# Performance work log

Hardware: AMD Instinct MI355X
Metric: run time of the kernel (lower is better)

## Reference

```python
import jax, jax.numpy as jnp
import numpy as np

DIM = 2048
N_HEADS = 16
HEAD_DIM = DIM // N_HEADS
MAX_SEQ_LEN = 2048
ROPE_THETA = 32.0
EPS = 1e-6


def _precompute_freqs_1d(dim, max_seq_len, theta):
    freqs = theta ** (-np.arange(0, dim, 2, dtype=np.float32) / dim)  # [dim/2]
    pos = np.arange(max_seq_len, dtype=np.float32)                    # [S]
    ang = pos[:, None] * freqs[None, :]                               # [S, dim/2]
    return jnp.asarray(np.cos(ang)), jnp.asarray(np.sin(ang))


def _rms_norm(x, w):
    # x: [..., d]
    inv = jax.lax.rsqrt(jnp.mean(x * x, axis=-1, keepdims=True) + EPS)
    return x * inv * w


def setup_inputs() -> dict:
    key = jax.random.key(0)
    k1, k2, k3 = jax.random.split(key, 3)
    bsz, seq_len = 4, 2048
    x = jax.random.normal(k1, (bsz, seq_len, DIM), dtype=jnp.float32)
    w_qkv = jax.random.normal(k2, (3 * DIM, DIM), dtype=jnp.float32) * (DIM ** -0.5)
    w_proj = jax.random.normal(k3, (DIM, DIM), dtype=jnp.float32) * (DIM ** -0.5)
    q_norm_w = jnp.ones((HEAD_DIM,), dtype=jnp.float32)
    k_norm_w = jnp.ones((HEAD_DIM,), dtype=jnp.float32)
    return {"x": x, "w_qkv": w_qkv, "w_proj": w_proj,
            "q_norm_w": q_norm_w, "k_norm_w": k_norm_w}


def reference(x, w_qkv, w_proj, q_norm_w, k_norm_w):
    bsz, seq_len, dim = x.shape
    scale = HEAD_DIM ** -0.5

    # QKV projection (torch Linear: x @ W^T)
    qkv = jnp.einsum('bsd,ed->bse', x, w_qkv)  # [b, s, 3*dim]
    qkv = qkv.reshape(bsz, seq_len, 3, N_HEADS, HEAD_DIM).transpose(2, 0, 3, 1, 4)
    q, k, v = qkv[0], qkv[1], qkv[2]           # each [b, h, s, d]

    # Per-head RMSNorm on q, k
    q = _rms_norm(q, q_norm_w)
    k = _rms_norm(k, k_norm_w)

    # RoPE (half-split convention)
    cos, sin = _precompute_freqs_1d(HEAD_DIM, MAX_SEQ_LEN, ROPE_THETA)
    cos = cos[:seq_len][None, None]  # [1,1,s,d/2]
    sin = sin[:seq_len][None, None]
    q1, q2 = jnp.split(q, 2, axis=-1)
    k1, k2 = jnp.split(k, 2, axis=-1)
    q = jnp.concatenate([q1 * cos - q2 * sin, q2 * cos + q1 * sin], axis=-1)
    k = jnp.concatenate([k1 * cos - k2 * sin, k2 * cos + k1 * sin], axis=-1)

    # Scaled dot-product attention (no mask, eval-mode: no dropout)
    scores = jnp.einsum('bhqd,bhkd->bhqk', q, k) * scale
    attn = jax.nn.softmax(scores, axis=-1)
    y = jnp.einsum('bhqk,bhkd->bhqd', attn, v)

    # Merge heads + output projection
    y = y.transpose(0, 2, 1, 3).reshape(bsz, seq_len, dim)
    return jnp.einsum('bsd,ed->bse', y, w_proj)
```

## Files before the change

### kernel.cpp

```cpp
#include <hip/hip_runtime.h>
#include <hip/hip_bf16.h>

#define BSZ 4
#define SEQ 2048
#define DIM 2048
#define NH 16
#define HD 128
#define QK_LD 4096
#define SCALE 0.08838834764831845f
#define SC2 0.12751742910198f

typedef __attribute__((ext_vector_type(8))) short bf16x8;
typedef __attribute__((ext_vector_type(4))) float f32x4;

#define GLDS16(g, l)                                                           \
  __builtin_amdgcn_global_load_lds(                                           \
      (const __attribute__((address_space(1))) void*)(g),                     \
      (__attribute__((address_space(3))) void*)(l), 16, 0, 0)

__device__ inline short f2b(float f) {
  __hip_bfloat16 h = __float2bfloat16(f);
  short s;
  __builtin_memcpy(&s, &h, 2);
  return s;
}

__device__ inline void stage16(const float* gp, __hip_bfloat16* lp) {
  float4 q0 = ((const float4*)gp)[0], q1 = ((const float4*)gp)[1];
  float4 q2 = ((const float4*)gp)[2], q3 = ((const float4*)gp)[3];
  bf16x8 v0, v1;
  v0[0] = f2b(q0.x); v0[1] = f2b(q0.y); v0[2] = f2b(q0.z); v0[3] = f2b(q0.w);
  v0[4] = f2b(q1.x); v0[5] = f2b(q1.y); v0[6] = f2b(q1.z); v0[7] = f2b(q1.w);
  v1[0] = f2b(q2.x); v1[1] = f2b(q2.y); v1[2] = f2b(q2.z); v1[3] = f2b(q2.w);
  v1[4] = f2b(q3.x); v1[5] = f2b(q3.y); v1[6] = f2b(q3.z); v1[7] = f2b(q3.w);
  *(bf16x8*)lp = v0;
  *(bf16x8*)(lp + 8) = v1;
}

__device__ inline char* out_slice(void* outv, int b, int fl) {
  return (char*)outv + (size_t)b * (size_t)SEQ * DIM * (fl ? 2u : 4u);
}

__global__ __launch_bounds__(256)
void detect_canon(const unsigned int* __restrict__ wbits,
                  const void* __restrict__ qw, const void* __restrict__ kw,
                  __hip_bfloat16* __restrict__ qwb,
                  __hip_bfloat16* __restrict__ kwb, int* __restrict__ flag) {
  __shared__ int cnt;
  const int t = threadIdx.x;
  if (t == 0) cnt = 0;
  __syncthreads();
  int local = 0;
  for (int i = 0; i < 4; ++i) {
    unsigned int e = (wbits[t * 4 + i] >> 7) & 0xFF;
    if (e >= 96 && e < 160) local++;
  }
  atomicAdd(&cnt, local);
  __syncthreads();
  const int f = (cnt >= 768) ? 1 : 0;
  if (t == 0) *flag = f;
  if (t < 128)
    qwb[t] = f ? ((const __hip_bfloat16*)qw)[t]
               : __float2bfloat16(((const float*)qw)[t]);
  else
    kwb[t - 128] = f ? ((const __hip_bfloat16*)kw)[t - 128]
                     : __float2bfloat16(((const float*)kw)[t - 128]);
}

__global__ __launch_bounds__(256)
void convert_bf16(const void* __restrict__ in, __hip_bfloat16* __restrict__ out,
                  const int* __restrict__ flag) {
  const int fl = *flag;
  long i = ((long)blockIdx.x * 256 + threadIdx.x) * 8;
  if (fl) {
    *(float4*)(out + i) = *(const float4*)((const __hip_bfloat16*)in + i);
  } else {
    const float* p = (const float*)in + i;
    float4 a = ((const float4*)p)[0], b = ((const float4*)p)[1];
    bf16x8 o;
    o[0] = f2b(a.x); o[1] = f2b(a.y); o[2] = f2b(a.z); o[3] = f2b(a.w);
    o[4] = f2b(b.x); o[5] = f2b(b.y); o[6] = f2b(b.z); o[7] = f2b(b.w);
    *(bf16x8*)(out + i) = o;
  }
}


__global__ __launch_bounds__(256)
void gemm_qkv_full(const __hip_bfloat16* __restrict__ A,
                   const __hip_bfloat16* __restrict__ B,
                   __hip_bfloat16* __restrict__ qk, void* __restrict__ outv,
                   const int* __restrict__ flag) {
  __shared__ __hip_bfloat16 As[128 * 32];
  __shared__ __hip_bfloat16 Bs[128 * 32];
  const int t = threadIdx.x, wave = t >> 6, lane = t & 63;
  const int quad = lane >> 4, l16 = lane & 15;
  const int wm = (wave & 1) * 64, wn = (wave >> 1) * 64;
  const long bm = (long)blockIdx.x * 128, bn = (long)blockIdx.y * 128;
  const int fl = *flag;

  f32x4 acc[4][4] = {};
  for (int k0 = 0; k0 < DIM; k0 += 32) {
    __syncthreads();
    for (int i = 0; i < 2; ++i) {
      int c = wave * 64 + lane + i * 256;
      int row = c >> 2, kc = c & 3;
      GLDS16(A + (bm + row) * DIM + k0 + kc * 8, As + (wave * 64 + i * 256) * 8);
      GLDS16(B + (bn + row) * DIM + k0 + kc * 8, Bs + (wave * 64 + i * 256) * 8);
    }
    __syncthreads();
    bf16x8 aF[4], bF[4];
    for (int mt = 0; mt < 4; ++mt)
      aF[mt] = *(const bf16x8*)(As + (wm + mt * 16 + l16) * 32 + quad * 8);
    for (int nt = 0; nt < 4; ++nt)
      bF[nt] = *(const bf16x8*)(Bs + (wn + nt * 16 + l16) * 32 + quad * 8);
    for (int mt = 0; mt < 4; ++mt)
      for (int nt = 0; nt < 4; ++nt)
        acc[mt][nt] = __builtin_amdgcn_mfma_f32_16x16x32_bf16(
            aF[mt], bF[nt], acc[mt][nt], 0, 0, 0);
  }

  if (bn < 4096) {
    for (int mt = 0; mt < 4; ++mt) {
      long gr = bm + wm + mt * 16 + quad * 4;
      for (int nt = 0; nt < 4; ++nt) {
        long gc = bn + wn + nt * 16 + l16;
        for (int r = 0; r < 4; ++r)
          qk[(gr + r) * QK_LD + gc] = __float2bfloat16(acc[mt][nt][r]);
      }
    }
  } else {
    for (int mt = 0; mt < 4; ++mt) {
      long gr = bm + wm + mt * 16 + quad * 4;
      __hip_bfloat16* vtb = (__hip_bfloat16*)out_slice(outv, (int)(gr >> 11), fl);
      long s = gr & 2047;
      for (int nt = 0; nt < 4; ++nt) {
        long col = bn - 4096 + wn + nt * 16 + l16;
        for (int r = 0; r < 4; ++r)
          vtb[col * SEQ + s + r] = __float2bfloat16(acc[mt][nt][r]);
      }
    }
  }
}

__global__ __launch_bounds__(256)
void gemm_proj_full(const __hip_bfloat16* __restrict__ A,
                    const __hip_bfloat16* __restrict__ B,
                    void* __restrict__ outv, const int* __restrict__ flag) {
  __shared__ __hip_bfloat16 As[128 * 32];
  __shared__ __hip_bfloat16 Bs[128 * 32];
  const int t = threadIdx.x, wave = t >> 6, lane = t & 63;
  const int quad = lane >> 4, l16 = lane & 15;
  const int wm = (wave & 1) * 64, wn = (wave >> 1) * 64;
  const long bm = (long)blockIdx.x * 128, bn = (long)blockIdx.y * 128;
  const int fl = *flag;

  f32x4 acc[4][4] = {};
  for (int k0 = 0; k0 < DIM; k0 += 32) {
    __syncthreads();
    for (int i = 0; i < 2; ++i) {
      int c = wave * 64 + lane + i * 256;
      int row = c >> 2, kc = c & 3;
      GLDS16(A + (bm + row) * QK_LD + k0 + kc * 8, As + (wave * 64 + i * 256) * 8);
      GLDS16(B + (bn + row) * DIM + k0 + kc * 8, Bs + (wave * 64 + i * 256) * 8);
    }
    __syncthreads();
    bf16x8 aF[4], bF[4];
    for (int mt = 0; mt < 4; ++mt)
      aF[mt] = *(const bf16x8*)(As + (wm + mt * 16 + l16) * 32 + quad * 8);
    for (int nt = 0; nt < 4; ++nt)
      bF[nt] = *(const bf16x8*)(Bs + (wn + nt * 16 + l16) * 32 + quad * 8);
    for (int mt = 0; mt < 4; ++mt)
      for (int nt = 0; nt < 4; ++nt)
        acc[mt][nt] = __builtin_amdgcn_mfma_f32_16x16x32_bf16(
            aF[mt], bF[nt], acc[mt][nt], 0, 0, 0);
  }

  for (int mt = 0; mt < 4; ++mt) {
    long gr = bm + wm + mt * 16 + quad * 4;
    for (int nt = 0; nt < 4; ++nt) {
      long gc = bn + wn + nt * 16 + l16;
      for (int r = 0; r < 4; ++r) {
        long idx = (gr + r) * DIM + gc;
        if (fl) ((__hip_bfloat16*)outv)[idx] = __float2bfloat16(acc[mt][nt][r]);
        else    ((float*)outv)[idx] = acc[mt][nt][r];
      }
    }
  }
}


__global__ __launch_bounds__(256)
void gemm_qkv(const void* __restrict__ xin, const void* __restrict__ win,
              __hip_bfloat16* __restrict__ qk, void* __restrict__ outv,
              const int* __restrict__ flag, int b) {
  __shared__ __hip_bfloat16 As[128 * 32];
  __shared__ __hip_bfloat16 Bs[128 * 32];
  const int t = threadIdx.x, wave = t >> 6, lane = t & 63;
  const int quad = lane >> 4, l16 = lane & 15;
  const int wm = (wave & 1) * 64, wn = (wave >> 1) * 64;
  const long bm = (long)blockIdx.x * 128, bn = (long)blockIdx.y * 128;
  const int fl = *flag;
  const __hip_bfloat16* Ab = (const __hip_bfloat16*)xin + (long)b * SEQ * DIM;
  const __hip_bfloat16* Bb = (const __hip_bfloat16*)win;
  const float* Af = (const float*)xin + (long)b * SEQ * DIM;
  const float* Bf = (const float*)win;

  f32x4 acc[4][4] = {};
  for (int k0 = 0; k0 < DIM; k0 += 32) {
    __syncthreads();
    if (fl) {
      for (int i = 0; i < 2; ++i) {
        int c = wave * 64 + lane + i * 256;
        int row = c >> 2, kc = c & 3;
        GLDS16(Ab + (bm + row) * DIM + k0 + kc * 8, As + (wave * 64 + i * 256) * 8);
        GLDS16(Bb + (bn + row) * DIM + k0 + kc * 8, Bs + (wave * 64 + i * 256) * 8);
      }
    } else {
      int row = t >> 1, cb = k0 + (t & 1) * 16;
      stage16(Af + (bm + row) * DIM + cb, As + t * 16);
      stage16(Bf + (bn + row) * DIM + cb, Bs + t * 16);
    }
    __syncthreads();
    bf16x8 aF[4], bF[4];
    for (int mt = 0; mt < 4; ++mt)
      aF[mt] = *(const bf16x8*)(As + (wm + mt * 16 + l16) * 32 + quad * 8);
    for (int nt = 0; nt < 4; ++nt)
      bF[nt] = *(const bf16x8*)(Bs + (wn + nt * 16 + l16) * 32 + quad * 8);
    for (int mt = 0; mt < 4; ++mt)
      for (int nt = 0; nt < 4; ++nt)
        acc[mt][nt] = __builtin_amdgcn_mfma_f32_16x16x32_bf16(
            aF[mt], bF[nt], acc[mt][nt], 0, 0, 0);
  }

  if (bn < 4096) {
    for (int mt = 0; mt < 4; ++mt) {
      long gr = bm + wm + mt * 16 + quad * 4;
      for (int nt = 0; nt < 4; ++nt) {
        long gc = bn + wn + nt * 16 + l16;
        for (int r = 0; r < 4; ++r)
          qk[(gr + r) * QK_LD + gc] = __float2bfloat16(acc[mt][nt][r]);
      }
    }
  } else {
    __hip_bfloat16* vtb = (__hip_bfloat16*)out_slice(outv, b, fl);
    for (int mt = 0; mt < 4; ++mt) {
      long gr = bm + wm + mt * 16 + quad * 4;
      for (int nt = 0; nt < 4; ++nt) {
        long col = bn - 4096 + wn + nt * 16 + l16;
        for (int r = 0; r < 4; ++r)
          vtb[col * SEQ + gr + r] = __float2bfloat16(acc[mt][nt][r]);
      }
    }
  }
}

__global__ __launch_bounds__(256)
void gemm_proj(const __hip_bfloat16* __restrict__ A, const void* __restrict__ win,
               void* __restrict__ outv, const int* __restrict__ flag, int b) {
  __shared__ __hip_bfloat16 As[128 * 32];
  __shared__ __hip_bfloat16 Bs[128 * 32];
  const int t = threadIdx.x, wave = t >> 6, lane = t & 63;
  const int quad = lane >> 4, l16 = lane & 15;
  const int wm = (wave & 1) * 64, wn = (wave >> 1) * 64;
  const long bm = (long)blockIdx.x * 128, bn = (long)blockIdx.y * 128;
  const int fl = *flag;
  const __hip_bfloat16* Bb = (const __hip_bfloat16*)win;
  const float* Bf = (const float*)win;

  f32x4 acc[4][4] = {};
  for (int k0 = 0; k0 < DIM; k0 += 32) {
    __syncthreads();
    for (int i = 0; i < 2; ++i) {
      int c = wave * 64 + lane + i * 256;
      int row = c >> 2, kc = c & 3;
      GLDS16(A + (bm + row) * QK_LD + k0 + kc * 8, As + (wave * 64 + i * 256) * 8);
    }
    if (fl) {
      for (int i = 0; i < 2; ++i) {
        int c = wave * 64 + lane + i * 256;
        int row = c >> 2, kc = c & 3;
        GLDS16(Bb + (bn + row) * DIM + k0 + kc * 8, Bs + (wave * 64 + i * 256) * 8);
      }
    } else {
      int row = t >> 1, cb = k0 + (t & 1) * 16;
      stage16(Bf + (bn + row) * DIM + cb, Bs + t * 16);
    }
    __syncthreads();
    bf16x8 aF[4], bF[4];
    for (int mt = 0; mt < 4; ++mt)
      aF[mt] = *(const bf16x8*)(As + (wm + mt * 16 + l16) * 32 + quad * 8);
    for (int nt = 0; nt < 4; ++nt)
      bF[nt] = *(const bf16x8*)(Bs + (wn + nt * 16 + l16) * 32 + quad * 8);
    for (int mt = 0; mt < 4; ++mt)
      for (int nt = 0; nt < 4; ++nt)
        acc[mt][nt] = __builtin_amdgcn_mfma_f32_16x16x32_bf16(
            aF[mt], bF[nt], acc[mt][nt], 0, 0, 0);
  }

  char* Cb = out_slice(outv, b, fl);
  for (int mt = 0; mt < 4; ++mt) {
    long gr = bm + wm + mt * 16 + quad * 4;
    for (int nt = 0; nt < 4; ++nt) {
      long gc = bn + wn + nt * 16 + l16;
      for (int r = 0; r < 4; ++r) {
        long idx = (gr + r) * DIM + gc;
        if (fl) ((__hip_bfloat16*)Cb)[idx] = __float2bfloat16(acc[mt][nt][r]);
        else    ((float*)Cb)[idx] = acc[mt][nt][r];
      }
    }
  }
}


__global__ __launch_bounds__(256)
void norm_rope(__hip_bfloat16* __restrict__ qk,
               const __hip_bfloat16* __restrict__ qwb,
               const __hip_bfloat16* __restrict__ kwb) {
  const int wave = threadIdx.x >> 6, lane = threadIdx.x & 63;
  const int gid = blockIdx.x * 4 + wave;
  const int h = gid & 15, tt = (gid >> 4) & 1, row = gid >> 5;
  const int s = row & 2047;

  __hip_bfloat16* p = qk + (long)row * QK_LD + tt * DIM + h * HD;
  unsigned int u = ((const unsigned int*)p)[lane];

  unsigned int x = (unsigned int)__shfl((int)u, lane >> 1);
  unsigned int y = (unsigned int)__shfl((int)u, 32 + (lane >> 1));
  float v1 = __uint_as_float((lane & 1) ? (x & 0xFFFF0000u) : (x << 16));
  float v2 = __uint_as_float((lane & 1) ? (y & 0xFFFF0000u) : (y << 16));

  float ss = v1 * v1 + v2 * v2;
  for (int off = 1; off < 64; off <<= 1) ss += __shfl_xor(ss, off);
  float inv = rsqrtf(ss * (1.0f / 128.0f) + 1e-6f);

  const __hip_bfloat16* w = tt ? kwb : qwb;
  float n1 = v1 * inv * __bfloat162float(w[lane]);
  float n2 = v2 * inv * __bfloat162float(w[lane + 64]);

  float freq = exp2f(-5.0f * (float)lane * (1.0f / 64.0f));
  float ang = (float)s * freq;
  float c = cosf(ang), sn = sinf(ang);
  float r1 = n1 * c - n2 * sn;
  float r2 = n2 * c + n1 * sn;

  float z1lo = __shfl(r1, (2 * lane) & 63), z2lo = __shfl(r2, (2 * lane) & 63);
  float z1hi = __shfl(r1, (2 * lane + 1) & 63), z2hi = __shfl(r2, (2 * lane + 1) & 63);
  float lo = (lane < 32) ? z1lo : z2lo;
  float hi = (lane < 32) ? z1hi : z2hi;
  unsigned int ou = (unsigned int)(unsigned short)f2b(lo) |
                    ((unsigned int)(unsigned short)f2b(hi) << 16);
  ((unsigned int*)p)[lane] = ou;
}

__global__ __launch_bounds__(512)
void flash_attn(__hip_bfloat16* __restrict__ qkbase, void* __restrict__ outv,
                const int* __restrict__ flag, int b0) {
  __shared__ __hip_bfloat16 Ks[4 * 64 * 32];
  __shared__ __hip_bfloat16 Vs[2 * 128 * 32];
  __shared__ __hip_bfloat16 Ps[8][2 * 16 * 32];

  const int t = threadIdx.x, wave = t >> 6, lane = t & 63;
  const int quad = lane >> 4, l16 = lane & 15;
  const int swz = (quad ^ ((l16 >> 1) & 3)) * 8;
  const int q0 = blockIdx.x * 128, h = blockIdx.y;
  const int b = b0 + blockIdx.z;
  const int fl = *flag;
  __hip_bfloat16* qk = qkbase + (long)blockIdx.z * SEQ * QK_LD;
  __hip_bfloat16* Qg = qk + h * HD;
  const __hip_bfloat16* Kg = Qg + DIM;
  const __hip_bfloat16* Vt =
      (const __hip_bfloat16*)out_slice(outv, b, fl) + (long)h * HD * SEQ;

  bf16x8 aQ[4];
#pragma unroll
  for (int ks = 0; ks < 4; ++ks)
    aQ[ks] = *(const bf16x8*)(Qg +
        (long)(q0 + wave * 16 + l16) * QK_LD + ks * 32 + quad * 8);

  f32x4 oacc[8] = {};
  float m_run[4], l_run[4];
#pragma unroll
  for (int r = 0; r < 4; ++r) { m_run[r] = -1e30f; l_run[r] = 0.0f; }

  for (int j0 = 0; j0 < SEQ; j0 += 64) {
    __syncthreads();
#pragma unroll
    for (int i = 0; i < 2; ++i) {
      int f = t + i * 512;
      int kk = f & 3, row = (f >> 2) & 63, ks = f >> 8;
      GLDS16(Kg + (long)(j0 + row) * QK_LD + ks * 32 + (kk ^ ((row >> 1) & 3)) * 8,
             Ks + (t + i * 512) * 8);
    }
#pragma unroll
    for (int i = 0; i < 2; ++i) {
      int f = t + i * 512;
      int kk = f & 3, dimr = (f >> 2) & 127, ks2 = f >> 9;
      GLDS16(Vt + (long)dimr * SEQ + j0 + ks2 * 32 + (kk ^ ((dimr >> 1) & 3)) * 8,
             Vs + (t + i * 512) * 8);
    }
    __syncthreads();

    f32x4 sacc[4] = {};
#pragma unroll
    for (int ks = 0; ks < 4; ++ks)
#pragma unroll
      for (int nt = 0; nt < 4; ++nt) {
        bf16x8 bK = *(const bf16x8*)(Ks + (ks * 64 + nt * 16 + l16) * 32 + swz);
        sacc[nt] = __builtin_amdgcn_mfma_f32_16x16x32_bf16(
            aQ[ks], bK, sacc[nt], 0, 0, 0);
      }

    __hip_bfloat16* pw = &Ps[wave][0];
#pragma unroll
    for (int r = 0; r < 4; ++r) {
      float p0 = sacc[0][r] * SC2, p1 = sacc[1][r] * SC2;
      float p2 = sacc[2][r] * SC2, p3 = sacc[3][r] * SC2;
      float mx = fmaxf(fmaxf(p0, p1), fmaxf(p2, p3));
      for (int off = 1; off < 16; off <<= 1)
        mx = fmaxf(mx, __shfl_xor(mx, off));
      if (__any(mx > m_run[r] + 8.0f)) {
        float mnew = fmaxf(m_run[r], mx);
        float alpha = exp2f(m_run[r] - mnew);
        m_run[r] = mnew;
        l_run[r] *= alpha;
#pragma unroll
        for (int n = 0; n < 8; ++n) oacc[n][r] *= alpha;
      }
      float m = m_run[r];
      float e0 = exp2f(p0 - m), e1 = exp2f(p1 - m);
      float e2 = exp2f(p2 - m), e3 = exp2f(p3 - m);
      l_run[r] += (e0 + e1) + (e2 + e3);
      int rbase = (quad * 4 + r) * 32;
      int sc = (((quad * 4 + r) >> 1) & 3) << 3;
      pw[rbase + (l16 ^ sc)] = __float2bfloat16(e0);
      pw[rbase + ((l16 + 16) ^ sc)] = __float2bfloat16(e1);
      pw[512 + rbase + (l16 ^ sc)] = __float2bfloat16(e2);
      pw[512 + rbase + ((l16 + 16) ^ sc)] = __float2bfloat16(e3);
    }

#pragma unroll
    for (int ks2 = 0; ks2 < 2; ++ks2) {
      bf16x8 aP = *(const bf16x8*)(pw + (ks2 * 16 + l16) * 32 + swz);
#pragma unroll
      for (int n = 0; n < 8; ++n) {
        bf16x8 bV = *(const bf16x8*)(Vs + (ks2 * 128 + n * 16 + l16) * 32 + swz);
        oacc[n] = __builtin_amdgcn_mfma_f32_16x16x32_bf16(
            aP, bV, oacc[n], 0, 0, 0);
      }
    }
  }

#pragma unroll
  for (int r = 0; r < 4; ++r) {
    float l = l_run[r];
    for (int off = 1; off < 16; off <<= 1) l += __shfl_xor(l, off);
    float rl = 1.0f / l;
    long s = q0 + wave * 16 + quad * 4 + r;
    for (int n = 0; n < 8; ++n)
      qk[s * QK_LD + h * HD + n * 16 + l16] =
          __float2bfloat16(oacc[n][r] * rl);
  }
}

extern "C" void kernel_launch(void* const* d_in, const int* in_sizes, int n_in,
                              void* d_out, int out_size, void* d_ws, size_t ws_size,
                              hipStream_t stream) {
  int* flag = (int*)d_ws;
  __hip_bfloat16* qwb = (__hip_bfloat16*)((char*)d_ws + 64);
  __hip_bfloat16* kwb = qwb + 128;
  char* base = (char*)d_ws + 1024;

  detect_canon<<<1, 256, 0, stream>>>((const unsigned int*)d_in[1], d_in[3],
                                      d_in[4], qwb, kwb, flag);

  const size_t MB = 1024ull * 1024ull;
  const size_t NEED_A = 1024 + 128 * MB;

  if (ws_size >= NEED_A) {
    __hip_bfloat16* xb     = (__hip_bfloat16*)base;
    __hip_bfloat16* wqkvb  = (__hip_bfloat16*)(base + 32 * MB);
    __hip_bfloat16* wprojb = (__hip_bfloat16*)(base + 56 * MB);
    __hip_bfloat16* qk     = (__hip_bfloat16*)(base + 64 * MB);

    convert_bf16<<<(BSZ * SEQ * DIM) / 2048, 256, 0, stream>>>(d_in[0], xb, flag);
    convert_bf16<<<(3 * DIM * DIM) / 2048, 256, 0, stream>>>(d_in[1], wqkvb, flag);
    convert_bf16<<<(DIM * DIM) / 2048, 256, 0, stream>>>(d_in[2], wprojb, flag);

    gemm_qkv_full<<<dim3((BSZ * SEQ) / 128, (3 * DIM) / 128), 256, 0, stream>>>(
        xb, wqkvb, qk, d_out, flag);
    norm_rope<<<(BSZ * SEQ * 2 * NH) / 4, 256, 0, stream>>>(qk, qwb, kwb);
    flash_attn<<<dim3(SEQ / 128, NH, BSZ), 512, 0, stream>>>(qk, d_out, flag, 0);
    gemm_proj_full<<<dim3((BSZ * SEQ) / 128, DIM / 128), 256, 0, stream>>>(
        qk, wprojb, d_out, flag);
  } else {
    __hip_bfloat16* qk = (__hip_bfloat16*)base;
    for (int b = 0; b < BSZ; ++b) {
      gemm_qkv<<<dim3(SEQ / 128, (3 * DIM) / 128), 256, 0, stream>>>(
          d_in[0], d_in[1], qk, d_out, flag, b);
      norm_rope<<<(SEQ * 2 * NH) / 4, 256, 0, stream>>>(qk, qwb, kwb);
      flash_attn<<<dim3(SEQ / 128, NH, 1), 512, 0, stream>>>(qk, d_out, flag, b);
      gemm_proj<<<dim3(SEQ / 128, DIM / 128), 256, 0, stream>>>(
          qk, d_in[2], d_out, flag, b);
    }
  }
}
```

Before: 868.6 us.

## Keep softmax probabilities in registers via transposed QK MFMA and remap GEMM blocks across XCDs

```diff
diff --git a/kernel.cpp b/kernel.cpp
--- a/kernel.cpp
+++ b/kernel.cpp
@@ -39,6 +39,15 @@
 
 __device__ inline char* out_slice(void* outv, int b, int fl) {
   return (char*)outv + (size_t)b * (size_t)SEQ * DIM * (fl ? 2u : 4u);
+}
+
+__device__ inline void xcd_remap(long& bm, long& bn) {
+  int nwg = gridDim.x * gridDim.y;
+  int lin = blockIdx.y * gridDim.x + blockIdx.x;
+  int cpx = nwg >> 3;
+  lin = (lin & 7) * cpx + (lin >> 3);
+  bm = (long)(lin % gridDim.x) * 128;
+  bn = (long)(lin / gridDim.x) * 128;
 }
 
 __global__ __launch_bounds__(256)
@@ -95,7 +104,8 @@
   const int t = threadIdx.x, wave = t >> 6, lane = t & 63;
   const int quad = lane >> 4, l16 = lane & 15;
   const int wm = (wave & 1) * 64, wn = (wave >> 1) * 64;
-  const long bm = (long)blockIdx.x * 128, bn = (long)blockIdx.y * 128;
+  long bm, bn;
+  xcd_remap(bm, bn);
   const int fl = *flag;
 
   f32x4 acc[4][4] = {};
@@ -151,7 +161,8 @@
   const int t = threadIdx.x, wave = t >> 6, lane = t & 63;
   const int quad = lane >> 4, l16 = lane & 15;
   const int wm = (wave & 1) * 64, wn = (wave >> 1) * 64;
-  const long bm = (long)blockIdx.x * 128, bn = (long)blockIdx.y * 128;
+  long bm, bn;
+  xcd_remap(bm, bn);
   const int fl = *flag;
 
   f32x4 acc[4][4] = {};
@@ -357,7 +368,6 @@
                 const int* __restrict__ flag, int b0) {
   __shared__ __hip_bfloat16 Ks[4 * 64 * 32];
   __shared__ __hip_bfloat16 Vs[2 * 128 * 32];
-  __shared__ __hip_bfloat16 Ps[8][2 * 16 * 32];
 
   const int t = threadIdx.x, wave = t >> 6, lane = t & 63;
   const int quad = lane >> 4, l16 = lane & 15;
@@ -371,6 +381,10 @@
   const __hip_bfloat16* Vt =
       (const __hip_bfloat16*)out_slice(outv, b, fl) + (long)h * HD * SEQ;
 
+  const int srcA = ((lane >> 4) & 1) * 32 + l16;
+  const int srcB = srcA + 16;
+  const bool hiq = (quad >= 2);
+
   bf16x8 aQ[4];
 #pragma unroll
   for (int ks = 0; ks < 4; ++ks)
@@ -378,9 +392,7 @@
         (long)(q0 + wave * 16 + l16) * QK_LD + ks * 32 + quad * 8);
 
   f32x4 oacc[8] = {};
-  float m_run[4], l_run[4];
-#pragma unroll
-  for (int r = 0; r < 4; ++r) { m_run[r] = -1e30f; l_run[r] = 0.0f; }
+  float m_run = -1e30f, l_run = 0.0f;
 
   for (int j0 = 0; j0 < SEQ; j0 += 64) {
     __syncthreads();
@@ -407,40 +419,62 @@
       for (int nt = 0; nt < 4; ++nt) {
         bf16x8 bK = *(const bf16x8*)(Ks + (ks * 64 + nt * 16 + l16) * 32 + swz);
         sacc[nt] = __builtin_amdgcn_mfma_f32_16x16x32_bf16(
-            aQ[ks], bK, sacc[nt], 0, 0, 0);
-      }
-
-    __hip_bfloat16* pw = &Ps[wave][0];
-#pragma unroll
-    for (int r = 0; r < 4; ++r) {
-      float p0 = sacc[0][r] * SC2, p1 = sacc[1][r] * SC2;
-      float p2 = sacc[2][r] * SC2, p3 = sacc[3][r] * SC2;
-      float mx = fmaxf(fmaxf(p0, p1), fmaxf(p2, p3));
-      for (int off = 1; off < 16; off <<= 1)
-        mx = fmaxf(mx, __shfl_xor(mx, off));
-      if (__any(mx > m_run[r] + 8.0f)) {
-        float mnew = fmaxf(m_run[r], mx);
-        float alpha = exp2f(m_run[r] - mnew);
-        m_run[r] = mnew;
-        l_run[r] *= alpha;
-#pragma unroll
-        for (int n = 0; n < 8; ++n) oacc[n][r] *= alpha;
-      }
-      float m = m_run[r];
-      float e0 = exp2f(p0 - m), e1 = exp2f(p1 - m);
-      float e2 = exp2f(p2 - m), e3 = exp2f(p3 - m);
-      l_run[r] += (e0 + e1) + (e2 + e3);
-      int rbase = (quad * 4 + r) * 32;
-      int sc = (((quad * 4 + r) >> 1) & 3) << 3;
-      pw[rbase + (l16 ^ sc)] = __float2bfloat16(e0);
-      pw[rbase + ((l16 + 16) ^ sc)] = __float2bfloat16(e1);
-      pw[512 + rbase + (l16 ^ sc)] = __float2bfloat16(e2);
-      pw[512 + rbase + ((l16 + 16) ^ sc)] = __float2bfloat16(e3);
-    }
-
+            bK, aQ[ks], sacc[nt], 0, 0, 0);
+      }
+
+    float p[16];
+#pragma unroll
+    for (int nt = 0; nt < 4; ++nt)
+#pragma unroll
+      for (int r = 0; r < 4; ++r) p[nt * 4 + r] = sacc[nt][r] * SC2;
+    float mx = p[0];
+#pragma unroll
+    for (int i = 1; i < 16; ++i) mx = fmaxf(mx, p[i]);
+    mx = fmaxf(mx, __shfl_xor(mx, 16));
+    mx = fmaxf(mx, __shfl_xor(mx, 32));
+    if (__any(mx > m_run + 8.0f)) {
+      float mnew = fmaxf(m_run, mx);
+      float alpha = exp2f(m_run - mnew);
+      m_run = mnew;
+      l_run *= alpha;
+#pragma unroll
+      for (int r = 0; r < 4; ++r) {
+        float ar = __shfl(alpha, quad * 20 + r);
+#pragma unroll
+        for (int n = 0; n < 8; ++n) oacc[n][r] *= ar;
+      }
+    }
+    unsigned int W[4][2];
+    float sum = 0.0f;
+#pragma unroll
+    for (int nt = 0; nt < 4; ++nt) {
+      float e0 = exp2f(p[nt * 4 + 0] - m_run), e1 = exp2f(p[nt * 4 + 1] - m_run);
+      float e2 = exp2f(p[nt * 4 + 2] - m_run), e3 = exp2f(p[nt * 4 + 3] - m_run);
+      sum += (e0 + e1) + (e2 + e3);
+      W[nt][0] = (unsigned int)(unsigned short)f2b(e0) |
+                 ((unsigned int)(unsigned short)f2b(e1) << 16);
+      W[nt][1] = (unsigned int)(unsigned short)f2b(e2) |
+                 ((unsigned int)(unsigned short)f2b(e3) << 16);
+    }
+    l_run += sum;
+
+    union { unsigned int u[4]; bf16x8 v; } ap[2];
 #pragma unroll
     for (int ks2 = 0; ks2 < 2; ++ks2) {
-      bf16x8 aP = *(const bf16x8*)(pw + (ks2 * 16 + l16) * 32 + swz);
+#pragma unroll
+      for (int hh = 0; hh < 2; ++hh) {
+        unsigned int lo0 = (unsigned int)__shfl((int)W[2 * ks2][hh], srcA);
+        unsigned int hi0 = (unsigned int)__shfl((int)W[2 * ks2 + 1][hh], srcA);
+        unsigned int lo1 = (unsigned int)__shfl((int)W[2 * ks2][hh], srcB);
+        unsigned int hi1 = (unsigned int)__shfl((int)W[2 * ks2 + 1][hh], srcB);
+        ap[ks2].u[hh] = hiq ? hi0 : lo0;
+        ap[ks2].u[2 + hh] = hiq ? hi1 : lo1;
+      }
+    }
+
+#pragma unroll
+    for (int ks2 = 0; ks2 < 2; ++ks2) {
+      bf16x8 aP = ap[ks2].v;
 #pragma unroll
       for (int n = 0; n < 8; ++n) {
         bf16x8 bV = *(const bf16x8*)(Vs + (ks2 * 128 + n * 16 + l16) * 32 + swz);
@@ -450,15 +484,17 @@
     }
   }
 
+  float l = l_run;
+  l += __shfl_xor(l, 16);
+  l += __shfl_xor(l, 32);
+  float rl = 1.0f / l;
 #pragma unroll
   for (int r = 0; r < 4; ++r) {
-    float l = l_run[r];
-    for (int off = 1; off < 16; off <<= 1) l += __shfl_xor(l, off);
-    float rl = 1.0f / l;
+    float rlr = __shfl(rl, quad * 20 + r);
     long s = q0 + wave * 16 + quad * 4 + r;
     for (int n = 0; n < 8; ++n)
       qk[s * QK_LD + h * HD + n * 16 + l16] =
-          __float2bfloat16(oacc[n][r] * rl);
+          __float2bfloat16(oacc[n][r] * rlr);
   }
 }
 
```

New measurement: 793.7 us. 1.09x faster.
